# Optimization experiments

Measured on AMD Instinct MI355X. Metric: run time of the kernel, lower is better.

Reference implementation:

```python
import jax, jax.numpy as jnp
import numpy as np

B, N, D, H, O = 8, 2048, 64, 64, 64
ALPHA = 2.0  # LeakyReLU negative slope per module default
NEG = -9e15


def _lin(x, W, b):
    # torch nn.Linear: y = x @ W.T + b, W is [out, in]
    return x @ W.T + b


def setup_inputs() -> dict:
    key = jax.random.key(0)
    ks = jax.random.split(key, 32)
    f32 = jnp.float32
    x = jax.random.normal(ks[0], (B, N, D), f32)
    adj = jax.random.randint(ks[1], (B, N, N), 0, 2).astype(f32)
    c = jax.random.normal(ks[2], (B, N, H), f32)
    h = jax.random.normal(ks[3], (B, N, H), f32)
    s = 0.1
    W = jax.random.normal(ks[4], (D, H), f32) * s           # GAT weight
    a = jax.random.normal(ks[5], (2 * H, 1), f32) * s       # GAT attention vector
    def lin(k, out_d, in_d):
        k1, k2 = jax.random.split(k)
        return (jax.random.normal(k1, (out_d, in_d), f32) * s,
                jax.random.normal(k2, (out_d,), f32) * s)
    Wf, bWf = lin(ks[6], H, H); Wi, bWi = lin(ks[7], H, H)
    Wo, bWo = lin(ks[8], H, H); Wc, bWc = lin(ks[9], H, H)
    Uf, bUf = lin(ks[10], H, D); Ui, bUi = lin(ks[11], H, D)
    Uo, bUo = lin(ks[12], H, D); Uc, bUc = lin(ks[13], H, D)
    Wout, bout = lin(ks[14], O, 2 * H)
    return dict(x=x, adj=adj, c=c, h=h, W=W, a=a,
                Wf=Wf, bWf=bWf, Wi=Wi, bWi=bWi, Wo=Wo, bWo=bWo, Wc=Wc, bWc=bWc,
                Uf=Uf, bUf=bUf, Ui=Ui, bUi=bUi, Uo=Uo, bUo=bUo, Uc=Uc, bUc=bUc,
                Wout=Wout, bout=bout)


def reference(x, adj, c, h, W, a,
              Wf, bWf, Wi, bWi, Wo, bWo, Wc, bWc,
              Uf, bUf, Ui, bUi, Uo, bUo, Uc, bUc,
              Wout, bout):
    # ---- GraphAttentionLayer (eval mode: dropout is identity) ----
    Wh = x @ W                                   # [B,N,H]
    # e[b,i,j] = leakyrelu(a[:H].Wh_i + a[H:].Wh_j) -- same math as the
    a_src = (Wh @ a[:H]).squeeze(-1)             # [B,N]
    a_dst = (Wh @ a[H:]).squeeze(-1)             # [B,N]
    e = jax.nn.leaky_relu(a_src[:, :, None] + a_dst[:, None, :], ALPHA)  # [B,N,N]
    att = jnp.where(adj > 0, e, NEG)
    att = jax.nn.softmax(att, axis=2)
    x_hidden = jax.nn.elu(att @ Wh)              # [B,N,H] (concat=True)
    # ---- LSTMLayer step ----
    f_t = jax.nn.sigmoid(_lin(h, Wf, bWf) + _lin(x, Uf, bUf))
    i_t = jax.nn.sigmoid(_lin(h, Wi, bWi) + _lin(x, Ui, bUi))
    o_t = jax.nn.sigmoid(_lin(h, Wo, bWo) + _lin(x, Uo, bUo))
    c_hat = jnp.tanh(_lin(h, Wc, bWc) + _lin(x, Uc, bUc))
    c_t = f_t * c + i_t * c_hat
    h_t = o_t * jax.nn.relu(c_t)                 # gate = nn.ReLU() default
    total = jnp.concatenate([x_hidden, h_t], axis=2)  # [B,N,2H]
    output = jax.nn.relu(_lin(total, Wout, bout))     # [B,N,O]
    return (output, h_t, c_t)
```

## Files before the change

### kernel.cpp

```cpp
#include <hip/hip_runtime.h>
#include <math.h>

#define B_ 8
#define N_ 2048
#define NT_ (B_*N_)
#define OUTSZ (NT_*64)

#define WS_ASRC  0
#define WS_ADST  (WS_ASRC + NT_)
#define WS_GMAX  (WS_ADST + NT_)
#define WS_WT    (WS_GMAX + 32)
#define WS_BB    (WS_WT + 128*256)
#define WS_WOT   (WS_BB + 256)
#define WS_PD    (WS_WOT + 128*64)
#define WS_PN    (WS_PD + 8*NT_)

typedef float f32x4 __attribute__((ext_vector_type(4)));
typedef __bf16 bf16x8 __attribute__((ext_vector_type(8)));
typedef __bf16 bf16x4 __attribute__((ext_vector_type(4)));

__device__ __forceinline__ float lrelu2(float x) { return x > 0.f ? x : 2.f * x; }
__device__ __forceinline__ float f4get(const float4& v, int k) { return k==0?v.x:(k==1?v.y:(k==2?v.z:v.w)); }

__global__ __launch_bounds__(256) void k1_wh(const float* __restrict__ x, const float* __restrict__ W,
                                             const float* __restrict__ a, float* __restrict__ ws,
                                             __bf16* __restrict__ whT,
                                             const float* Wf, const float* Wi, const float* Wo, const float* Wc,
                                             const float* Uf, const float* Ui, const float* Uo, const float* Uc,
                                             const float* bWf, const float* bWi, const float* bWo, const float* bWc,
                                             const float* bUf, const float* bUi, const float* bUo, const float* bUc,
                                             const float* Wout)
{
    __shared__ float xl[64 * 68];
    __shared__ float Wl[64 * 68];
    int t = threadIdx.x;
    if (blockIdx.x >= 256) {
        int idx = (blockIdx.x - 256) * 256 + t;
        if (idx < 128 * 256) {
            int k = idx >> 8, o = idx & 255;
            int g = o >> 6, u = o & 63;
            const float* Wg = (g == 0) ? Wf : (g == 1) ? Wi : (g == 2) ? Wo : Wc;
            const float* Ug = (g == 0) ? Uf : (g == 1) ? Ui : (g == 2) ? Uo : Uc;
            ws[WS_WT + idx] = (k < 64) ? Wg[u * 64 + k] : Ug[u * 64 + (k - 64)];
        } else if (idx < 128 * 256 + 256) {
            int o = idx - 128 * 256;
            int g = o >> 6, u = o & 63;
            const float* bW = (g == 0) ? bWf : (g == 1) ? bWi : (g == 2) ? bWo : bWc;
            const float* bU = (g == 0) ? bUf : (g == 1) ? bUi : (g == 2) ? bUo : bUc;
            ws[WS_BB + o] = bW[u] + bU[u];
        } else if (idx < 128 * 256 + 256 + 128 * 64) {
            int j = idx - (128 * 256 + 256);
            int k = j >> 6, u = j & 63;
            ws[WS_WOT + j] = Wout[u * 128 + k];
        }
        return;
    }
    int i0 = blockIdx.x * 64;
    #pragma unroll
    for (int it = 0; it < 4; ++it) {
        int f = t + 256 * it;
        int r = f >> 4, q = f & 15;
        *(float4*)&xl[r * 68 + q * 4] = *(const float4*)&x[i0 * 64 + f * 4];
        *(float4*)&Wl[r * 68 + q * 4] = *(const float4*)&W[f * 4];
    }
    __syncthreads();
    int cg = t & 15, rg = t >> 4;
    int c0 = cg * 4, r0 = rg * 4;
    float acc[4][4] = {};
    #pragma unroll
    for (int d0 = 0; d0 < 64; d0 += 4) {
        float4 wv[4], xv[4];
        #pragma unroll
        for (int k = 0; k < 4; ++k) wv[k] = *(float4*)&Wl[(d0 + k) * 68 + c0];
        #pragma unroll
        for (int ri = 0; ri < 4; ++ri) xv[ri] = *(float4*)&xl[(r0 + ri) * 68 + d0];
        #pragma unroll
        for (int ri = 0; ri < 4; ++ri)
            #pragma unroll
            for (int k = 0; k < 4; ++k) {
                float xs = f4get(xv[ri], k);
                acc[ri][0] += xs * wv[k].x; acc[ri][1] += xs * wv[k].y;
                acc[ri][2] += xs * wv[k].z; acc[ri][3] += xs * wv[k].w;
            }
    }
    int b = i0 >> 11;
    int rowb0 = (i0 & 2047) + r0;
    #pragma unroll
    for (int cj = 0; cj < 4; ++cj) {
        bf16x4 v;
        v[0] = (__bf16)acc[0][cj]; v[1] = (__bf16)acc[1][cj];
        v[2] = (__bf16)acc[2][cj]; v[3] = (__bf16)acc[3][cj];
        *(bf16x4*)&whT[((size_t)(b * 64 + c0 + cj)) * N_ + rowb0] = v;
    }
    float4 a0 = *(const float4*)&a[c0];
    float4 a1 = *(const float4*)&a[64 + c0];
    float wmax = -3.0e38f;
    #pragma unroll
    for (int ri = 0; ri < 4; ++ri) {
        int row = i0 + r0 + ri;
        float s0 = acc[ri][0]*a0.x + acc[ri][1]*a0.y + acc[ri][2]*a0.z + acc[ri][3]*a0.w;
        float s1 = acc[ri][0]*a1.x + acc[ri][1]*a1.y + acc[ri][2]*a1.z + acc[ri][3]*a1.w;
        #pragma unroll
        for (int m = 1; m < 16; m <<= 1) { s0 += __shfl_xor(s0, m, 64); s1 += __shfl_xor(s1, m, 64); }
        if (cg == 0) { ws[WS_ASRC + row] = s0; ws[WS_ADST + row] = s1; }
        float m16 = fmaxf(s1, __shfl_xor(s1, 16, 64));
        m16 = fmaxf(m16, __shfl_xor(m16, 32, 64));
        wmax = fmaxf(wmax, m16);
    }
    if ((t & 63) == 0) {
        unsigned u = __float_as_uint(wmax);
        unsigned e = (u & 0x80000000u) ? ~u : (u | 0x80000000u);
        atomicMax(((unsigned*)&ws[WS_GMAX]) + b, e);
    }
}

__global__ __launch_bounds__(256) void k2v5(const float* __restrict__ adj,
                                            const __bf16* __restrict__ whT,
                                            float* __restrict__ ws)
{
    __shared__ float lsa[2][4][16][68];
    __shared__ float lsd[2][4][16];
    int tid = threadIdx.x;
    int lane = tid & 63, w = tid >> 6;
    int r = lane & 15, g = lane >> 4;
    int jr = blockIdx.x & 7;
    int rslab = blockIdx.x >> 3;
    int b = rslab >> 4;
    int row_base = rslab * 128;
    int jbeg = jr * 256 + w * 64;

    unsigned ge = ((const unsigned*)&ws[WS_GMAX])[b];
    float gmax = (ge & 0x80000000u) ? __uint_as_float(ge & 0x7FFFFFFFu) : __uint_as_float(~ge);

    bf16x8 bfr[2][4];
    #pragma unroll
    for (int ks = 0; ks < 2; ++ks)
        #pragma unroll
        for (int n = 0; n < 4; ++n)
            bfr[ks][n] = *(const bf16x8*)&whT[(size_t)(b * 64 + n * 16 + r) * N_ + jbeg + ks * 32 + g * 8];
    float ejr[2][8];
    #pragma unroll
    for (int ks = 0; ks < 2; ++ks) {
        float4 d0 = *(const float4*)&ws[WS_ADST + b * N_ + jbeg + ks * 32 + g * 8];
        float4 d1 = *(const float4*)&ws[WS_ADST + b * N_ + jbeg + ks * 32 + g * 8 + 4];
        ejr[ks][0]=__expf(d0.x); ejr[ks][1]=__expf(d0.y); ejr[ks][2]=__expf(d0.z); ejr[ks][3]=__expf(d0.w);
        ejr[ks][4]=__expf(d1.x); ejr[ks][5]=__expf(d1.y); ejr[ks][6]=__expf(d1.z); ejr[ks][7]=__expf(d1.w);
    }

    float4 av[2][4];
    float asv[2];

#define LDT(T, S)                                                                  \
    {                                                                              \
        int row0_ = row_base + (T) * 16;                                           \
        const float* ap_ = &adj[(size_t)(row0_ + r) * N_ + jbeg];                  \
        av[S][0] = *(const float4*)&ap_[g * 8];                                    \
        av[S][1] = *(const float4*)&ap_[g * 8 + 4];                                \
        av[S][2] = *(const float4*)&ap_[32 + g * 8];                               \
        av[S][3] = *(const float4*)&ap_[32 + g * 8 + 4];                           \
        asv[S] = ws[WS_ASRC + row0_ + r];                                          \
    }

    LDT(0, 0);

    #pragma unroll
    for (int t = 0; t < 8; ++t) {
        const int s = t & 1;
        if (t + 1 < 8) { LDT(t + 1, (t + 1) & 1); }
        float as = asv[s];
        float M  = lrelu2(as + gmax);
        float c1 = __expf(as - M);
        float c2 = __expf(2.f * as - M);
        float thr = __expf(-as);
        f32x4 acc[4] = {{0.f,0.f,0.f,0.f},{0.f,0.f,0.f,0.f},{0.f,0.f,0.f,0.f},{0.f,0.f,0.f,0.f}};
        float dsum = 0.f;
        #pragma unroll
        for (int ks = 0; ks < 2; ++ks) {
            bf16x8 af;
            float ds_ = 0.f;
            #pragma unroll
            for (int e = 0; e < 8; ++e) {
                float avv = f4get(e < 4 ? av[s][ks * 2] : av[s][ks * 2 + 1], e & 3);
                float E = ejr[ks][e];
                float p = (E > thr) ? c1 * E : (c2 * E) * E;
                p = (avv > 0.f) ? p : 0.f;
                ds_ += p;
                af[e] = (__bf16)p;
            }
            dsum += ds_;
            #pragma unroll
            for (int n = 0; n < 4; ++n)
                acc[n] = __builtin_amdgcn_mfma_f32_16x16x32_bf16(af, bfr[ks][n], acc[n], 0, 0, 0);
        }
        dsum += __shfl_xor(dsum, 16, 64);
        dsum += __shfl_xor(dsum, 32, 64);
        #pragma unroll
        for (int n = 0; n < 4; ++n)
            #pragma unroll
            for (int i = 0; i < 4; ++i)
                lsa[s][w][g * 4 + i][n * 16 + r] = acc[n][i];
        if (g == 0) lsd[s][w][r] = dsum;
        asm volatile("s_waitcnt lgkmcnt(0)" ::: "memory");
        __builtin_amdgcn_s_barrier();
        asm volatile("" ::: "memory");
        {
            int rl = tid >> 4, h0 = (tid & 15) * 4;
            float4 sv = make_float4(0.f, 0.f, 0.f, 0.f);
            #pragma unroll
            for (int w2 = 0; w2 < 4; ++w2) {
                float4 q = *(const float4*)&lsa[s][w2][rl][h0];
                sv.x += q.x; sv.y += q.y; sv.z += q.z; sv.w += q.w;
            }
            int row0 = row_base + t * 16;
            *(float4*)&ws[WS_PN + ((size_t)jr * NT_ + row0 + rl) * 64 + h0] = sv;
            if (tid < 16)
                ws[WS_PD + jr * NT_ + row0 + tid] =
                    lsd[s][0][tid] + lsd[s][1][tid] + lsd[s][2][tid] + lsd[s][3][tid];
        }
    }
#undef LDT
}

__global__ __launch_bounds__(256) void k3_lstm(const float* __restrict__ x, const float* __restrict__ c,
                                               const float* __restrict__ h, const float* __restrict__ ws,
                                               float* __restrict__ out)
{
    __shared__ float Al[16 * 132];
    __shared__ float gl[16 * 260];
    int t = threadIdx.x;
    int base = blockIdx.x * 16;
    {
        int r = t >> 4, k0 = (t & 15) * 8;
        const float* src = (k0 < 64) ? &h[(base + r) * 64 + k0] : &x[(base + r) * 64 + (k0 - 64)];
        *(float4*)&Al[r * 132 + k0]     = *(const float4*)&src[0];
        *(float4*)&Al[r * 132 + k0 + 4] = *(const float4*)&src[4];
    }
    __syncthreads();
    int og = t & 63, rg = t >> 6;
    int o0 = og * 4;
    const float* WT = &ws[WS_WT];
    float acc[4][4] = {};
    #pragma unroll
    for (int k0 = 0; k0 < 128; k0 += 4) {
        float4 wv[4], av[4];
        #pragma unroll
        for (int kk = 0; kk < 4; ++kk) wv[kk] = *(const float4*)&WT[(k0 + kk) * 256 + o0];
        #pragma unroll
        for (int rr = 0; rr < 4; ++rr) av[rr] = *(float4*)&Al[(rg + 4 * rr) * 132 + k0];
        #pragma unroll
        for (int rr = 0; rr < 4; ++rr)
            #pragma unroll
            for (int kk = 0; kk < 4; ++kk) {
                float as = f4get(av[rr], kk);
                acc[rr][0] += as * wv[kk].x; acc[rr][1] += as * wv[kk].y;
                acc[rr][2] += as * wv[kk].z; acc[rr][3] += as * wv[kk].w;
            }
    }
    float4 bbv = *(const float4*)&ws[WS_BB + o0];
    #pragma unroll
    for (int rr = 0; rr < 4; ++rr) {
        int r = rg + 4 * rr;
        *(float4*)&gl[r * 260 + o0] = make_float4(acc[rr][0] + bbv.x, acc[rr][1] + bbv.y,
                                                  acc[rr][2] + bbv.z, acc[rr][3] + bbv.w);
    }
    __syncthreads();
    int u = t & 63, rq = t >> 6;
    #pragma unroll
    for (int pp = 0; pp < 4; ++pp) {
        int r = rq + 4 * pp;
        float gf = gl[r * 260 + u];
        float gi = gl[r * 260 + 64 + u];
        float go = gl[r * 260 + 128 + u];
        float gc = gl[r * 260 + 192 + u];
        float fg = 1.f / (1.f + __expf(-gf));
        float ig = 1.f / (1.f + __expf(-gi));
        float oo = 1.f / (1.f + __expf(-go));
        float ch = tanhf(gc);
        float cv = c[(base + r) * 64 + u];
        float ct = fg * cv + ig * ch;
        float ht = oo * fmaxf(ct, 0.f);
        out[OUTSZ + (base + r) * 64 + u] = ht;
        out[2 * OUTSZ + (base + r) * 64 + u] = ct;
    }
}

__global__ __launch_bounds__(256) void k5_out(const float* __restrict__ ws, const float* __restrict__ bout,
                                              float* __restrict__ out)
{
    __shared__ float Al[64 * 132];
    int t = threadIdx.x;
    int base = blockIdx.x * 64;
    const float* ht = &out[OUTSZ];
    #pragma unroll
    for (int it = 0; it < 8; ++it) {
        int f = t + 256 * it;
        int r = f >> 5, q = f & 31;
        int k0 = q * 4;
        int row = base + r;
        float4 v;
        if (k0 < 64) {
            float4 s = make_float4(0.f, 0.f, 0.f, 0.f);
            float d = 0.f;
            #pragma unroll
            for (int jr = 0; jr < 8; ++jr) {
                float4 p = *(const float4*)&ws[WS_PN + ((size_t)jr * NT_ + row) * 64 + k0];
                s.x += p.x; s.y += p.y; s.z += p.z; s.w += p.w;
                d += ws[WS_PD + jr * NT_ + row];
            }
            float inv = 1.f / d;
            v.x = s.x * inv; v.x = v.x > 0.f ? v.x : expm1f(v.x);
            v.y = s.y * inv; v.y = v.y > 0.f ? v.y : expm1f(v.y);
            v.z = s.z * inv; v.z = v.z > 0.f ? v.z : expm1f(v.z);
            v.w = s.w * inv; v.w = v.w > 0.f ? v.w : expm1f(v.w);
        } else {
            v = *(const float4*)&ht[(size_t)row * 64 + (k0 - 64)];
        }
        *(float4*)&Al[r * 132 + k0] = v;
    }
    __syncthreads();
    int cg = t & 15, rgG = t >> 4;
    int c0 = cg * 4, r0 = rgG * 4;
    const float* WT = &ws[WS_WOT];
    float acc[4][4] = {};
    #pragma unroll
    for (int k0 = 0; k0 < 128; k0 += 4) {
        float4 wv[4], av[4];
        #pragma unroll
        for (int kk = 0; kk < 4; ++kk) wv[kk] = *(const float4*)&WT[(k0 + kk) * 64 + c0];
        #pragma unroll
        for (int ri = 0; ri < 4; ++ri) av[ri] = *(float4*)&Al[(r0 + ri) * 132 + k0];
        #pragma unroll
        for (int ri = 0; ri < 4; ++ri)
            #pragma unroll
            for (int kk = 0; kk < 4; ++kk) {
                float as = f4get(av[ri], kk);
                acc[ri][0] += as * wv[kk].x; acc[ri][1] += as * wv[kk].y;
                acc[ri][2] += as * wv[kk].z; acc[ri][3] += as * wv[kk].w;
            }
    }
    float4 bo = *(const float4*)&bout[c0];
    #pragma unroll
    for (int ri = 0; ri < 4; ++ri) {
        int row = base + r0 + ri;
        float4 o;
        o.x = fmaxf(acc[ri][0] + bo.x, 0.f);
        o.y = fmaxf(acc[ri][1] + bo.y, 0.f);
        o.z = fmaxf(acc[ri][2] + bo.z, 0.f);
        o.w = fmaxf(acc[ri][3] + bo.w, 0.f);
        *(float4*)&out[row * 64 + c0] = o;
    }
}

extern "C" void kernel_launch(void* const* d_in, const int* in_sizes, int n_in,
                              void* d_out, int out_size, void* d_ws, size_t ws_size,
                              hipStream_t stream)
{
    const float* x    = (const float*)d_in[0];
    const float* adj  = (const float*)d_in[1];
    const float* c    = (const float*)d_in[2];
    const float* h    = (const float*)d_in[3];
    const float* W    = (const float*)d_in[4];
    const float* a    = (const float*)d_in[5];
    const float* Wf   = (const float*)d_in[6];
    const float* bWf  = (const float*)d_in[7];
    const float* Wi   = (const float*)d_in[8];
    const float* bWi  = (const float*)d_in[9];
    const float* Wo   = (const float*)d_in[10];
    const float* bWo  = (const float*)d_in[11];
    const float* Wc   = (const float*)d_in[12];
    const float* bWc  = (const float*)d_in[13];
    const float* Uf   = (const float*)d_in[14];
    const float* bUf  = (const float*)d_in[15];
    const float* Ui   = (const float*)d_in[16];
    const float* bUi  = (const float*)d_in[17];
    const float* Uo   = (const float*)d_in[18];
    const float* bUo  = (const float*)d_in[19];
    const float* Uc   = (const float*)d_in[20];
    const float* bUc  = (const float*)d_in[21];
    const float* Wout = (const float*)d_in[22];
    const float* bout = (const float*)d_in[23];
    float* out = (float*)d_out;
    float* ws  = (float*)d_ws;
    __bf16* whT = (__bf16*)out;

    hipMemsetAsync((void*)(ws + WS_GMAX), 0, 32 * sizeof(float), stream);

    k1_wh<<<417, 256, 0, stream>>>(x, W, a, ws, whT,
                                   Wf, Wi, Wo, Wc, Uf, Ui, Uo, Uc,
                                   bWf, bWi, bWo, bWc, bUf, bUi, bUo, bUc, Wout);
    k3_lstm<<<NT_ / 16, 256, 0, stream>>>(x, c, h, ws, out);
    k2v5<<<1024, 256, 0, stream>>>(adj, whT, ws);
    k5_out<<<NT_ / 64, 256, 0, stream>>>(ws, bout, out);
}
```

Baseline: 102.7 us.

## Restructure attention kernel so each block owns full rows and finalizes softmax-ELU

The attention-aggregation kernel now assigns each block 16 rows across the full 2048 columns, with each wave covering 512 columns. Before, each block handled a 128-row slab over a 256-column chunk. Partial numerators and denominators reduce in shared memory once at the end, and the kernel applies normalization and ELU directly. This removes the 8-way partial-sum workspace writes and the re-reduction in the output kernel. exp(a_dst) is precomputed in the Wh kernel instead of per block. The trade-off is that Wh and exp tiles are now streamed from global memory every iteration rather than held in registers, and there are 1024 blocks instead of 1024 of a different shape.

Measured after the change: 107.8 us. 5.0% more time.

```diff
diff --git a/kernel.cpp b/kernel.cpp
--- a/kernel.cpp
+++ b/kernel.cpp
@@ -8,12 +8,12 @@
 
 #define WS_ASRC  0
 #define WS_ADST  (WS_ASRC + NT_)
-#define WS_GMAX  (WS_ADST + NT_)
+#define WS_EJ    (WS_ADST + NT_)
+#define WS_GMAX  (WS_EJ + NT_)
 #define WS_WT    (WS_GMAX + 32)
 #define WS_BB    (WS_WT + 128*256)
 #define WS_WOT   (WS_BB + 256)
-#define WS_PD    (WS_WOT + 128*64)
-#define WS_PN    (WS_PD + 8*NT_)
+#define WS_XH    (WS_WOT + 128*64)
 
 typedef float f32x4 __attribute__((ext_vector_type(4)));
 typedef __bf16 bf16x8 __attribute__((ext_vector_type(8)));
@@ -102,7 +102,11 @@
         float s1 = acc[ri][0]*a1.x + acc[ri][1]*a1.y + acc[ri][2]*a1.z + acc[ri][3]*a1.w;
         #pragma unroll
         for (int m = 1; m < 16; m <<= 1) { s0 += __shfl_xor(s0, m, 64); s1 += __shfl_xor(s1, m, 64); }
-        if (cg == 0) { ws[WS_ASRC + row] = s0; ws[WS_ADST + row] = s1; }
+        if (cg == 0) {
+            ws[WS_ASRC + row] = s0;
+            ws[WS_ADST + row] = s1;
+            ws[WS_EJ + row]   = __expf(s1);
+        }
         float m16 = fmaxf(s1, __shfl_xor(s1, 16, 64));
         m16 = fmaxf(m16, __shfl_xor(m16, 32, 64));
         wmax = fmaxf(wmax, m16);
@@ -114,111 +118,107 @@
     }
 }
 
-__global__ __launch_bounds__(256) void k2v5(const float* __restrict__ adj,
+__global__ __launch_bounds__(256) void k2v6(const float* __restrict__ adj,
                                             const __bf16* __restrict__ whT,
                                             float* __restrict__ ws)
 {
-    __shared__ float lsa[2][4][16][68];
-    __shared__ float lsd[2][4][16];
+    __shared__ float lsa[4][16][68];
+    __shared__ float lsd[4][16];
     int tid = threadIdx.x;
     int lane = tid & 63, w = tid >> 6;
     int r = lane & 15, g = lane >> 4;
-    int jr = blockIdx.x & 7;
-    int rslab = blockIdx.x >> 3;
-    int b = rslab >> 4;
-    int row_base = rslab * 128;
-    int jbeg = jr * 256 + w * 64;
+    int row0 = blockIdx.x * 16;
+    int b = row0 >> 11;
+    int jbeg = w * 512;
 
     unsigned ge = ((const unsigned*)&ws[WS_GMAX])[b];
     float gmax = (ge & 0x80000000u) ? __uint_as_float(ge & 0x7FFFFFFFu) : __uint_as_float(~ge);
-
-    bf16x8 bfr[2][4];
-    #pragma unroll
-    for (int ks = 0; ks < 2; ++ks)
-        #pragma unroll
-        for (int n = 0; n < 4; ++n)
-            bfr[ks][n] = *(const bf16x8*)&whT[(size_t)(b * 64 + n * 16 + r) * N_ + jbeg + ks * 32 + g * 8];
-    float ejr[2][8];
-    #pragma unroll
-    for (int ks = 0; ks < 2; ++ks) {
-        float4 d0 = *(const float4*)&ws[WS_ADST + b * N_ + jbeg + ks * 32 + g * 8];
-        float4 d1 = *(const float4*)&ws[WS_ADST + b * N_ + jbeg + ks * 32 + g * 8 + 4];
-        ejr[ks][0]=__expf(d0.x); ejr[ks][1]=__expf(d0.y); ejr[ks][2]=__expf(d0.z); ejr[ks][3]=__expf(d0.w);
-        ejr[ks][4]=__expf(d1.x); ejr[ks][5]=__expf(d1.y); ejr[ks][6]=__expf(d1.z); ejr[ks][7]=__expf(d1.w);
-    }
+    float as = ws[WS_ASRC + row0 + r];
+    float M  = lrelu2(as + gmax);
+    float c1 = __expf(as - M);
+    float c2 = __expf(2.f * as - M);
+    float thr = __expf(-as);
+
+    const float* aprow = &adj[(size_t)(row0 + r) * N_ + jbeg];
+    const float* ejp   = &ws[WS_EJ + b * N_ + jbeg];
+    const __bf16* bb   = &whT[(size_t)(b * 64 + r) * N_ + jbeg];
+
+    f32x4 acc0 = {0.f,0.f,0.f,0.f}, acc1 = {0.f,0.f,0.f,0.f};
+    f32x4 acc2 = {0.f,0.f,0.f,0.f}, acc3 = {0.f,0.f,0.f,0.f};
+    float dsum = 0.f;
 
     float4 av[2][4];
-    float asv[2];
-
-#define LDT(T, S)                                                                  \
-    {                                                                              \
-        int row0_ = row_base + (T) * 16;                                           \
-        const float* ap_ = &adj[(size_t)(row0_ + r) * N_ + jbeg];                  \
-        av[S][0] = *(const float4*)&ap_[g * 8];                                    \
-        av[S][1] = *(const float4*)&ap_[g * 8 + 4];                                \
-        av[S][2] = *(const float4*)&ap_[32 + g * 8];                               \
-        av[S][3] = *(const float4*)&ap_[32 + g * 8 + 4];                           \
-        asv[S] = ws[WS_ASRC + row0_ + r];                                          \
-    }
-
-    LDT(0, 0);
-
+#define LDA(T, S)                                                \
+    {                                                            \
+        const float* ap_ = aprow + (T) * 64;                     \
+        av[S][0] = *(const float4*)&ap_[g * 8];                  \
+        av[S][1] = *(const float4*)&ap_[g * 8 + 4];              \
+        av[S][2] = *(const float4*)&ap_[32 + g * 8];             \
+        av[S][3] = *(const float4*)&ap_[32 + g * 8 + 4];         \
+    }
+
+    LDA(0, 0);
     #pragma unroll
     for (int t = 0; t < 8; ++t) {
         const int s = t & 1;
-        if (t + 1 < 8) { LDT(t + 1, (t + 1) & 1); }
-        float as = asv[s];
-        float M  = lrelu2(as + gmax);
-        float c1 = __expf(as - M);
-        float c2 = __expf(2.f * as - M);
-        float thr = __expf(-as);
-        f32x4 acc[4] = {{0.f,0.f,0.f,0.f},{0.f,0.f,0.f,0.f},{0.f,0.f,0.f,0.f},{0.f,0.f,0.f,0.f}};
-        float dsum = 0.f;
+        if (t < 7) { LDA(t + 1, s ^ 1); }
+        int jj = t * 64;
         #pragma unroll
         for (int ks = 0; ks < 2; ++ks) {
+            float4 e0 = *(const float4*)&ejp[jj + ks * 32 + g * 8];
+            float4 e1 = *(const float4*)&ejp[jj + ks * 32 + g * 8 + 4];
+            bf16x8 b0 = *(const bf16x8*)&bb[jj + ks * 32 + g * 8];
+            bf16x8 b1 = *(const bf16x8*)&bb[16 * N_ + jj + ks * 32 + g * 8];
+            bf16x8 b2 = *(const bf16x8*)&bb[32 * N_ + jj + ks * 32 + g * 8];
+            bf16x8 b3 = *(const bf16x8*)&bb[48 * N_ + jj + ks * 32 + g * 8];
             bf16x8 af;
             float ds_ = 0.f;
             #pragma unroll
             for (int e = 0; e < 8; ++e) {
                 float avv = f4get(e < 4 ? av[s][ks * 2] : av[s][ks * 2 + 1], e & 3);
-                float E = ejr[ks][e];
+                float E = f4get(e < 4 ? e0 : e1, e & 3);
                 float p = (E > thr) ? c1 * E : (c2 * E) * E;
                 p = (avv > 0.f) ? p : 0.f;
                 ds_ += p;
                 af[e] = (__bf16)p;
             }
             dsum += ds_;
-            #pragma unroll
-            for (int n = 0; n < 4; ++n)
-                acc[n] = __builtin_amdgcn_mfma_f32_16x16x32_bf16(af, bfr[ks][n], acc[n], 0, 0, 0);
+            acc0 = __builtin_amdgcn_mfma_f32_16x16x32_bf16(af, b0, acc0, 0, 0, 0);
+            acc1 = __builtin_amdgcn_mfma_f32_16x16x32_bf16(af, b1, acc1, 0, 0, 0);
+            acc2 = __builtin_amdgcn_mfma_f32_16x16x32_bf16(af, b2, acc2, 0, 0, 0);
+            acc3 = __builtin_amdgcn_mfma_f32_16x16x32_bf16(af, b3, acc3, 0, 0, 0);
         }
-        dsum += __shfl_xor(dsum, 16, 64);
-        dsum += __shfl_xor(dsum, 32, 64);
-        #pragma unroll
-        for (int n = 0; n < 4; ++n)
-            #pragma unroll
-            for (int i = 0; i < 4; ++i)
-                lsa[s][w][g * 4 + i][n * 16 + r] = acc[n][i];
-        if (g == 0) lsd[s][w][r] = dsum;
-        asm volatile("s_waitcnt lgkmcnt(0)" ::: "memory");
-        __builtin_amdgcn_s_barrier();
-        asm volatile("" ::: "memory");
-        {
-            int rl = tid >> 4, h0 = (tid & 15) * 4;
-            float4 sv = make_float4(0.f, 0.f, 0.f, 0.f);
-            #pragma unroll
-            for (int w2 = 0; w2 < 4; ++w2) {
-                float4 q = *(const float4*)&lsa[s][w2][rl][h0];
-                sv.x += q.x; sv.y += q.y; sv.z += q.z; sv.w += q.w;
-            }
-            int row0 = row_base + t * 16;
-            *(float4*)&ws[WS_PN + ((size_t)jr * NT_ + row0 + rl) * 64 + h0] = sv;
-            if (tid < 16)
-                ws[WS_PD + jr * NT_ + row0 + tid] =
-                    lsd[s][0][tid] + lsd[s][1][tid] + lsd[s][2][tid] + lsd[s][3][tid];
+    }
+#undef LDA
+    dsum += __shfl_xor(dsum, 16, 64);
+    dsum += __shfl_xor(dsum, 32, 64);
+
+    #pragma unroll
+    for (int i = 0; i < 4; ++i) {
+        lsa[w][g * 4 + i][ 0 + r] = acc0[i];
+        lsa[w][g * 4 + i][16 + r] = acc1[i];
+        lsa[w][g * 4 + i][32 + r] = acc2[i];
+        lsa[w][g * 4 + i][48 + r] = acc3[i];
+    }
+    if (g == 0) lsd[w][r] = dsum;
+    __syncthreads();
+    {
+        int rl = tid >> 4, h0 = (tid & 15) * 4;
+        float4 sv = make_float4(0.f, 0.f, 0.f, 0.f);
+        #pragma unroll
+        for (int w2 = 0; w2 < 4; ++w2) {
+            float4 q = *(const float4*)&lsa[w2][rl][h0];
+            sv.x += q.x; sv.y += q.y; sv.z += q.z; sv.w += q.w;
         }
-    }
-#undef LDT
+        float dtot = lsd[0][rl] + lsd[1][rl] + lsd[2][rl] + lsd[3][rl];
+        float inv = 1.f / dtot;
+        float4 o;
+        o.x = sv.x * inv; o.x = o.x > 0.f ? o.x : expm1f(o.x);
+        o.y = sv.y * inv; o.y = o.y > 0.f ? o.y : expm1f(o.y);
+        o.z = sv.z * inv; o.z = o.z > 0.f ? o.z : expm1f(o.z);
+        o.w = sv.w * inv; o.w = o.w > 0.f ? o.w : expm1f(o.w);
+        *(float4*)&ws[WS_XH + (size_t)(row0 + rl) * 64 + h0] = o;
+    }
 }
 
 __global__ __launch_bounds__(256) void k3_lstm(const float* __restrict__ x, const float* __restrict__ c,
@@ -290,31 +290,16 @@
     __shared__ float Al[64 * 132];
     int t = threadIdx.x;
     int base = blockIdx.x * 64;
+    const float* xh = &ws[WS_XH];
     const float* ht = &out[OUTSZ];
     #pragma unroll
     for (int it = 0; it < 8; ++it) {
         int f = t + 256 * it;
         int r = f >> 5, q = f & 31;
         int k0 = q * 4;
-        int row = base + r;
         float4 v;
-        if (k0 < 64) {
-            float4 s = make_float4(0.f, 0.f, 0.f, 0.f);
-            float d = 0.f;
-            #pragma unroll
-            for (int jr = 0; jr < 8; ++jr) {
-                float4 p = *(const float4*)&ws[WS_PN + ((size_t)jr * NT_ + row) * 64 + k0];
-                s.x += p.x; s.y += p.y; s.z += p.z; s.w += p.w;
-                d += ws[WS_PD + jr * NT_ + row];
-            }
-            float inv = 1.f / d;
-            v.x = s.x * inv; v.x = v.x > 0.f ? v.x : expm1f(v.x);
-            v.y = s.y * inv; v.y = v.y > 0.f ? v.y : expm1f(v.y);
-            v.z = s.z * inv; v.z = v.z > 0.f ? v.z : expm1f(v.z);
-            v.w = s.w * inv; v.w = v.w > 0.f ? v.w : expm1f(v.w);
-        } else {
-            v = *(const float4*)&ht[(size_t)row * 64 + (k0 - 64)];
-        }
+        if (k0 < 64) v = *(const float4*)&xh[(size_t)(base + r) * 64 + k0];
+        else         v = *(const float4*)&ht[(size_t)(base + r) * 64 + (k0 - 64)];
         *(float4*)&Al[r * 132 + k0] = v;
     }
     __syncthreads();
@@ -389,6 +374,6 @@
                                    Wf, Wi, Wo, Wc, Uf, Ui, Uo, Uc,
                                    bWf, bWi, bWo, bWc, bUf, bUi, bUo, bUc, Wout);
     k3_lstm<<<NT_ / 16, 256, 0, stream>>>(x, c, h, ws, out);
-    k2v5<<<1024, 256, 0, stream>>>(adj, whT, ws);
+    k2v6<<<NT_ / 16, 256, 0, stream>>>(adj, whT, ws);
     k5_out<<<NT_ / 64, 256, 0, stream>>>(ws, bout, out);
 }
```

## Stage adjacency tiles through LDS with coalesced row loads and two-deep prefetch

Applied to the files above, without the earlier changes.

Adjacency rows are now read with fully coalesced row-contiguous float4 loads (each wave covers 4 rows across the 256-column slab), converted to bf16, and staged in a double-buffered LDS tile. Each MFMA lane then reads its fragment from LDS instead of doing strided per-lane global loads. Prefetch depth grows to two tiles ahead, and the row src scores are preloaded. The cost is an extra barrier per iteration plus LDS writes and reads, and the partial-sum buffer is now single-buffered.

New measurement: 102.0 us. No clear change (-0.6%).

```diff
diff --git a/kernel.cpp b/kernel.cpp
--- a/kernel.cpp
+++ b/kernel.cpp
@@ -114,12 +114,13 @@
     }
 }
 
-__global__ __launch_bounds__(256) void k2v5(const float* __restrict__ adj,
+__global__ __launch_bounds__(256) void k2v9(const float* __restrict__ adj,
                                             const __bf16* __restrict__ whT,
                                             float* __restrict__ ws)
 {
-    __shared__ float lsa[2][4][16][68];
-    __shared__ float lsd[2][4][16];
+    __shared__ __bf16 adjt[2][16][268];
+    __shared__ float lsa[4][16][68];
+    __shared__ float lsd[4][16];
     int tid = threadIdx.x;
     int lane = tid & 63, w = tid >> 6;
     int r = lane & 15, g = lane >> 4;
@@ -146,28 +147,43 @@
         ejr[ks][0]=__expf(d0.x); ejr[ks][1]=__expf(d0.y); ejr[ks][2]=__expf(d0.z); ejr[ks][3]=__expf(d0.w);
         ejr[ks][4]=__expf(d1.x); ejr[ks][5]=__expf(d1.y); ejr[ks][6]=__expf(d1.z); ejr[ks][7]=__expf(d1.w);
     }
-
-    float4 av[2][4];
-    float asv[2];
-
-#define LDT(T, S)                                                                  \
-    {                                                                              \
-        int row0_ = row_base + (T) * 16;                                           \
-        const float* ap_ = &adj[(size_t)(row0_ + r) * N_ + jbeg];                  \
-        av[S][0] = *(const float4*)&ap_[g * 8];                                    \
-        av[S][1] = *(const float4*)&ap_[g * 8 + 4];                                \
-        av[S][2] = *(const float4*)&ap_[32 + g * 8];                               \
-        av[S][3] = *(const float4*)&ap_[32 + g * 8 + 4];                           \
-        asv[S] = ws[WS_ASRC + row0_ + r];                                          \
-    }
-
-    LDT(0, 0);
+    float asv8[8];
+    #pragma unroll
+    for (int tt = 0; tt < 8; ++tt)
+        asv8[tt] = ws[WS_ASRC + row_base + tt * 16 + r];
+
+    f32x4 sreg[2][4];
+
+#define SLOAD(T, S)                                                                        \
+    {                                                                                      \
+        _Pragma("unroll")                                                                  \
+        for (int i = 0; i < 4; ++i)                                                        \
+            sreg[S][i] = *(const f32x4*)&adj[(size_t)(row_base + (T) * 16 + w * 4 + i) * N_ \
+                                             + jr * 256 + lane * 4];                       \
+    }
+#define SWRITE(T, S)                                                                       \
+    {                                                                                      \
+        _Pragma("unroll")                                                                  \
+        for (int i = 0; i < 4; ++i) {                                                      \
+            bf16x4 bv;                                                                     \
+            bv[0] = (__bf16)sreg[S][i][0]; bv[1] = (__bf16)sreg[S][i][1];                  \
+            bv[2] = (__bf16)sreg[S][i][2]; bv[3] = (__bf16)sreg[S][i][3];                  \
+            *(bf16x4*)&adjt[(T) & 1][w * 4 + i][lane * 4] = bv;                            \
+        }                                                                                  \
+    }
+
+    SLOAD(0, 0);
+    SWRITE(0, 0);
+    SLOAD(1, 1);
+    asm volatile("s_waitcnt lgkmcnt(0)" ::: "memory");
+    __builtin_amdgcn_s_barrier();
+    asm volatile("" ::: "memory");
 
     #pragma unroll
     for (int t = 0; t < 8; ++t) {
         const int s = t & 1;
-        if (t + 1 < 8) { LDT(t + 1, (t + 1) & 1); }
-        float as = asv[s];
+        if (t + 2 < 8) { SLOAD(t + 2, s); }
+        float as = asv8[t];
         float M  = lrelu2(as + gmax);
         float c1 = __expf(as - M);
         float c2 = __expf(2.f * as - M);
@@ -176,11 +192,12 @@
         float dsum = 0.f;
         #pragma unroll
         for (int ks = 0; ks < 2; ++ks) {
+            bf16x8 at = *(const bf16x8*)&adjt[s][r][w * 64 + ks * 32 + g * 8];
             bf16x8 af;
             float ds_ = 0.f;
             #pragma unroll
             for (int e = 0; e < 8; ++e) {
-                float avv = f4get(e < 4 ? av[s][ks * 2] : av[s][ks * 2 + 1], e & 3);
+                float avv = (float)at[e];
                 float E = ejr[ks][e];
                 float p = (E > thr) ? c1 * E : (c2 * E) * E;
                 p = (avv > 0.f) ? p : 0.f;
@@ -198,8 +215,9 @@
         for (int n = 0; n < 4; ++n)
             #pragma unroll
             for (int i = 0; i < 4; ++i)
-                lsa[s][w][g * 4 + i][n * 16 + r] = acc[n][i];
-        if (g == 0) lsd[s][w][r] = dsum;
+                lsa[w][g * 4 + i][n * 16 + r] = acc[n][i];
+        if (g == 0) lsd[w][r] = dsum;
+        if (t + 1 < 8) { SWRITE(t + 1, s ^ 1); }
         asm volatile("s_waitcnt lgkmcnt(0)" ::: "memory");
         __builtin_amdgcn_s_barrier();
         asm volatile("" ::: "memory");
@@ -208,17 +226,21 @@
             float4 sv = make_float4(0.f, 0.f, 0.f, 0.f);
             #pragma unroll
             for (int w2 = 0; w2 < 4; ++w2) {
-                float4 q = *(const float4*)&lsa[s][w2][rl][h0];
+                float4 q = *(const float4*)&lsa[w2][rl][h0];
                 sv.x += q.x; sv.y += q.y; sv.z += q.z; sv.w += q.w;
             }
             int row0 = row_base + t * 16;
             *(float4*)&ws[WS_PN + ((size_t)jr * NT_ + row0 + rl) * 64 + h0] = sv;
             if (tid < 16)
                 ws[WS_PD + jr * NT_ + row0 + tid] =
-                    lsd[s][0][tid] + lsd[s][1][tid] + lsd[s][2][tid] + lsd[s][3][tid];
+                    lsd[0][tid] + lsd[1][tid] + lsd[2][tid] + lsd[3][tid];
         }
-    }
-#undef LDT
+        asm volatile("s_waitcnt lgkmcnt(0)" ::: "memory");
+        __builtin_amdgcn_s_barrier();
+        asm volatile("" ::: "memory");
+    }
+#undef SLOAD
+#undef SWRITE
 }
 
 __global__ __launch_bounds__(256) void k3_lstm(const float* __restrict__ x, const float* __restrict__ c,
@@ -389,6 +411,6 @@
                                    Wf, Wi, Wo, Wc, Uf, Ui, Uo, Uc,
                                    bWf, bWi, bWo, bWc, bUf, bUi, bUo, bUc, Wout);
     k3_lstm<<<NT_ / 16, 256, 0, stream>>>(x, c, h, ws, out);
-    k2v5<<<1024, 256, 0, stream>>>(adj, whT, ws);
+    k2v9<<<1024, 256, 0, stream>>>(adj, whT, ws);
     k5_out<<<NT_ / 64, 256, 0, stream>>>(ws, bout, out);
 }
```
